# Optimization experiments

Measured on AMD Instinct MI355X. Metric: run time of the kernel, lower is better.

Reference implementation:

```python
import jax, jax.numpy as jnp
import numpy as np

EMB = 256
N_NODES = 100000
N_EDGES = 500000
N_REL = 10
REL_DIM = 64
HID = 128
HEADS = 4
HEAD_DIM = HID // HEADS


def setup_inputs() -> dict:
    key = jax.random.key(0)
    ks = jax.random.split(key, 16)
    s = lambda i, shape: jax.random.normal(ks[i], shape, dtype=jnp.float32) * 0.05
    return {
        "node_embeddings": jax.random.normal(ks[0], (N_NODES, EMB), dtype=jnp.float32),
        "edge_index": jax.random.randint(ks[1], (2, N_EDGES), 0, N_NODES),
        "relation_type": jax.random.randint(ks[2], (N_EDGES,), 0, N_REL),
        "rel_emb": s(3, (N_REL, REL_DIM)),
        "W_edge": s(4, (2 * EMB, HID)), "b_edge": jnp.zeros((HID,), jnp.float32),
        "W_q": s(5, (REL_DIM, HID)), "b_q": jnp.zeros((HID,), jnp.float32),
        "W_k": s(6, (HID, HID)), "b_k": jnp.zeros((HID,), jnp.float32),
        "W_v": s(7, (HID, HID)), "b_v": jnp.zeros((HID,), jnp.float32),
        "W_o1": s(8, (HID, HID)), "b_o1": jnp.zeros((HID,), jnp.float32),
        "W_o2": s(9, (HID, 1)), "b_o2": jnp.zeros((1,), jnp.float32),
    }


def reference(node_embeddings, edge_index, relation_type, rel_emb,
              W_edge, b_edge, W_q, b_q, W_k, b_k, W_v, b_v,
              W_o1, b_o1, W_o2, b_o2):
    # Gather endpoint features: [E, 2*EMB]
    src = node_embeddings[edge_index[0]]
    tgt = node_embeddings[edge_index[1]]
    edge_features = jnp.concatenate([src, tgt], axis=1)
    # Edge MLP (dropout is identity at eval): [E, HID]
    edge_hidden = jax.nn.relu(edge_features @ W_edge + b_edge)
    # Relation embedding lookup: [E, REL_DIM]
    rel = rel_emb[relation_type]
    E = edge_hidden.shape[0]
    Q = (rel @ W_q + b_q).reshape(E, HEADS, HEAD_DIM)
    K = (edge_hidden @ W_k + b_k).reshape(E, HEADS, HEAD_DIM)
    V = (edge_hidden @ W_v + b_v).reshape(E, HEADS, HEAD_DIM)
    scale = jnp.sqrt(jnp.float32(HEAD_DIM))
    scores = jnp.sum(Q * K, axis=-1) / scale          # [E, HEADS]
    attn = jax.nn.softmax(scores, axis=-1)            # softmax over heads
    attended = (attn[..., None] * V).reshape(E, HID)
    output = attended + edge_hidden
    # Output MLP: Linear->ReLU->Linear(1)
    h = jax.nn.relu(output @ W_o1 + b_o1)
    score = (h @ W_o2 + b_o2).squeeze(-1)             # [E]
    return score
```

## Files before the change

kernel.cpp:

```cpp
#include <hip/hip_runtime.h>

#define EMB   256
#define HID   128
#define RELD  64
#define NREL  10
#define TE    128
#define SHSTR 130

typedef __attribute__((ext_vector_type(8)))  short bf16x8;
typedef __attribute__((ext_vector_type(16))) float f32x16;

__device__ __forceinline__ float bf16_to_f32(unsigned short u) {
    union { unsigned int i; float f; } v;
    v.i = ((unsigned int)u) << 16;
    return v.f;
}

__device__ __forceinline__ unsigned short f32_to_bf16(float x) {
    union { unsigned int i; float f; } v;
    v.f = x;
    unsigned int b = v.i;
    unsigned int rounded = b + 0x7fffu + ((b >> 16) & 1u);
    return (unsigned short)(rounded >> 16);
}

template <bool F32>
__device__ __forceinline__ float ldx(const void* p, size_t i) {
    if (F32) return ((const float*)p)[i];
    return bf16_to_f32(((const unsigned short*)p)[i]);
}

__device__ __forceinline__ bool detect_f32(const void* nodeEmb) {
    const float* f = (const float*)nodeEmb;
    float x = f[(threadIdx.x & 63) * 997];
    bool sane = isfinite(x) && fabsf(x) < 1.0e6f;
    unsigned long long m = __ballot(sane);
    return __popcll(m) >= 48;
}

__device__ __forceinline__ void gload16(const void* g, void* l) {
    __builtin_amdgcn_global_load_lds(
        (const __attribute__((address_space(1))) unsigned int*)g,
        (__attribute__((address_space(3))) unsigned int*)l, 16, 0, 0);
}

#define WAITVL(n) asm volatile("s_waitcnt vmcnt(" #n ") lgkmcnt(0)" ::: "memory")

__device__ __forceinline__ void sbar() {
    __builtin_amdgcn_sched_barrier(0);
    __builtin_amdgcn_s_barrier();
    __builtin_amdgcn_sched_barrier(0);
}
__device__ __forceinline__ void bar_lds() {
    asm volatile("s_waitcnt lgkmcnt(0)" ::: "memory");
    sbar();
}

template <bool F32>
__device__ void prep_body(int vb, const void* W_edge, const void* W_k,
                          const void* W_v, const void* W_o1, const void* rel_emb,
                          const void* W_q, const void* b_q,
                          unsigned short* WTe, unsigned short* WTk,
                          unsigned short* WTv, unsigned short* WTo1, float* Qtab)
{
    if (vb < 448) {
        int idx = vb * 256 + threadIdx.x;
        if (idx < 65536) {
            int kc = idx >> 12, e = idx & 4095;
            int g = e >> 3, j = e & 7;
            int col = g & 127, kg = g >> 7;
            int k = kc * 32 + kg * 8 + j;
            WTe[idx] = f32_to_bf16(ldx<F32>(W_edge, (size_t)k * HID + col));
        } else if (idx < 65536 + 16384) {
            int i = idx - 65536;
            int kc = i >> 12, e = i & 4095;
            int g = e >> 3, j = e & 7;
            int col = g & 127, kg = (g >> 7) & 3;
            int k = kc * 32 + kg * 8 + j;
            WTk[i] = f32_to_bf16(ldx<F32>(W_k, (size_t)k * HID + col));
        } else if (idx < 65536 + 2 * 16384) {
            int i = idx - 65536 - 16384;
            int kc = i >> 12, e = i & 4095;
            int g = e >> 3, j = e & 7;
            int col = g & 127, kg = (g >> 7) & 3;
            int k = kc * 32 + kg * 8 + j;
            WTv[i] = f32_to_bf16(ldx<F32>(W_v, (size_t)k * HID + col));
        } else {
            int i = idx - 65536 - 2 * 16384;
            int kc = i >> 12, e = i & 4095;
            int g = e >> 3, j = e & 7;
            int col = g & 127, kg = (g >> 7) & 3;
            int k = kc * 32 + kg * 8 + j;
            WTo1[i] = f32_to_bf16(ldx<F32>(W_o1, (size_t)k * HID + col));
        }
    } else {
        const int t = threadIdx.x;
        const int c = t & (HID - 1);
        const int h = t >> 7;
        for (int r = h; r < NREL; r += 2) {
            float acc = 0.f;
            for (int d = 0; d < RELD; ++d)
                acc += ldx<F32>(rel_emb, r * RELD + d) * ldx<F32>(W_q, (size_t)d * HID + c);
            Qtab[r * HID + c] = acc + ldx<F32>(b_q, c);
        }
    }
}

__global__ void prep_kernel(const void* nodeEmb,
                            const void* W_edge, const void* W_k, const void* W_v,
                            const void* W_o1, const void* rel_emb, const void* W_q,
                            const void* b_q,
                            unsigned short* WTe, unsigned short* WTk,
                            unsigned short* WTv, unsigned short* WTo1, float* Qtab,
                            unsigned short* nodeBf16, int convBlocks,
                            unsigned long long nodeElems)
{
    bool f32 = detect_f32(nodeEmb);
    int b = blockIdx.x;
    if (b < convBlocks) {
        if (!f32) return;
        unsigned long long i = (unsigned long long)b * 2048ull + threadIdx.x * 8;
        if (i + 8 <= nodeElems) {
            const float* src = (const float*)nodeEmb + i;
            float4 f0 = *(const float4*)src;
            float4 f1 = *(const float4*)(src + 4);
            union { unsigned short us[8]; uint4 v; } pk;
            pk.us[0] = f32_to_bf16(f0.x); pk.us[1] = f32_to_bf16(f0.y);
            pk.us[2] = f32_to_bf16(f0.z); pk.us[3] = f32_to_bf16(f0.w);
            pk.us[4] = f32_to_bf16(f1.x); pk.us[5] = f32_to_bf16(f1.y);
            pk.us[6] = f32_to_bf16(f1.z); pk.us[7] = f32_to_bf16(f1.w);
            *(uint4*)(nodeBf16 + i) = pk.v;
        }
        return;
    }
    b -= convBlocks;
    if (f32) prep_body<true >(b, W_edge, W_k, W_v, W_o1, rel_emb, W_q, b_q,
                              WTe, WTk, WTv, WTo1, Qtab);
    else     prep_body<false>(b, W_edge, W_k, W_v, W_o1, rel_emb, W_q, b_q,
                              WTe, WTk, WTv, WTo1, Qtab);
}

struct __align__(16) Smem {
    unsigned short sHid[16 * SHSTR * 8];
    unsigned short SB[2][8192];
    float sQf[NREL * HID];
    float sBias[5 * HID];
    float sSc[TE][4];
    float sAttn[TE][4];
    float sPart[TE][2];
    int   sSrc[TE], sTgt[TE], sRel[TE];
};

__device__ __forceinline__ int shid_idx(int row, int k) {
    return (((k >> 3) * SHSTR + row) << 3) + (k & 7);
}

template <bool GBF16>
__device__ __forceinline__ bf16x8 loadA8(const void* row, int off) {
    if (GBF16) {
        return *(const bf16x8*)((const unsigned short*)row + off);
    } else {
        const float* p = (const float*)row + off;
        float4 f0 = *(const float4*)p;
        float4 f1 = *(const float4*)(p + 4);
        union { unsigned short us[8]; bf16x8 v; } pk;
        pk.us[0] = f32_to_bf16(f0.x); pk.us[1] = f32_to_bf16(f0.y);
        pk.us[2] = f32_to_bf16(f0.z); pk.us[3] = f32_to_bf16(f0.w);
        pk.us[4] = f32_to_bf16(f1.x); pk.us[5] = f32_to_bf16(f1.y);
        pk.us[6] = f32_to_bf16(f1.z); pk.us[7] = f32_to_bf16(f1.w);
        return pk.v;
    }
}

template <bool F32, bool GBF16>
__device__ void fused_body(
    Smem& sm,
    const void* gsrc, const int* edgeIdx, const int* relType,
    const unsigned short* WTe, const unsigned short* WTk,
    const unsigned short* WTv, const unsigned short* WTo1,
    const void* b_edge, const void* b_k, const void* b_v,
    const void* b_o1, const void* W_o2, const void* b_o2,
    const float* Qtab, void* outp, int E)
{
    const int t   = threadIdx.x;
    const int l   = t & 63;
    const int w   = t >> 6;
    const int c   = l & 31;
    const int h5  = l >> 5;
    const int rt  = w >> 1;
    const int cg2 = w & 1;
    const int bs  = blockIdx.x * TE;
    const int aRow = 32 * rt + c;

    if (t < TE) {
        int e = bs + t;
        if (e >= E) e = E - 1;
        if (e < 0)  e = 0;
        sm.sSrc[t] = edgeIdx[e];
        sm.sTgt[t] = edgeIdx[E + e];
        int r = relType[e];
        if (r < 0) r = 0;
        if (r >= NREL) r = NREL - 1;
        sm.sRel[t] = r;
    }
    for (int i = t; i < 5 * HID; i += 512) {
        int which = i >> 7, j = i & (HID - 1);
        float v = (which == 0) ? ldx<F32>(b_edge, j)
                : (which == 1) ? ldx<F32>(b_k, j)
                : (which == 2) ? ldx<F32>(b_v, j)
                : (which == 3) ? ldx<F32>(b_o1, j)
                               : ldx<F32>(W_o2, j);
        sm.sBias[i] = v;
    }
    for (int i = t; i < NREL * HID; i += 512)
        sm.sQf[i] = Qtab[i];
    __syncthreads();

    const void* rowSrc;
    const void* rowTgt;
    if (GBF16) {
        rowSrc = (const void*)((const unsigned short*)gsrc + (size_t)sm.sSrc[aRow] * EMB);
        rowTgt = (const void*)((const unsigned short*)gsrc + (size_t)sm.sTgt[aRow] * EMB);
    } else {
        rowSrc = (const void*)((const float*)gsrc + (size_t)sm.sSrc[aRow] * EMB);
        rowTgt = (const void*)((const float*)gsrc + (size_t)sm.sTgt[aRow] * EMB);
    }

    char* const ldsB0 = (char*)sm.SB[0] + w * 1024;
    char* const ldsB1 = (char*)sm.SB[1] + w * 1024;

    #define LOAD_A(k32, s) \
        loadA8<GBF16>(((k32) < 8) ? rowSrc : rowTgt, ((k32) & 7) * 32 + (s) * 16 + h5 * 8)
    #define STAGE_B64(WT, kc, buf)                                               \
    {                                                                            \
        gload16((WT) + (2 * (kc)    ) * 4096 + t * 8,                            \
                ((buf) ? ldsB1 : ldsB0));                                        \
        gload16((WT) + (2 * (kc) + 1) * 4096 + t * 8,                            \
                ((buf) ? ldsB1 : ldsB0) + 8192);                                 \
    }

    #define MFMA_AR64(slot, buf, accv)                                           \
    {                                                                            \
        const char* sb_ = (const char*)sm.SB[(buf)];                             \
        _Pragma("unroll")                                                        \
        for (int h_ = 0; h_ < 2; ++h_)                                           \
        _Pragma("unroll")                                                        \
        for (int s_ = 0; s_ < 2; ++s_) {                                         \
            _Pragma("unroll")                                                    \
            for (int ct_ = 0; ct_ < 2; ++ct_) {                                  \
                bf16x8 b_ = *(const bf16x8*)                                     \
                    (sb_ + h_ * 8192 +                                           \
                     ((s_ * 256 + h5 * 128 + 64 * cg2 + 32 * ct_ + c) << 4));    \
                accv[ct_] = __builtin_amdgcn_mfma_f32_32x32x16_bf16(             \
                                aR[slot][h_ * 2 + s_], b_, accv[ct_], 0, 0, 0);  \
            }                                                                    \
        }                                                                        \
    }

    #define MFMA_H64(kc, buf, accv)                                              \
    {                                                                            \
        const char* sb_ = (const char*)sm.SB[(buf)];                             \
        _Pragma("unroll")                                                        \
        for (int h_ = 0; h_ < 2; ++h_)                                           \
        _Pragma("unroll")                                                        \
        for (int s_ = 0; s_ < 2; ++s_) {                                         \
            bf16x8 a_ = *(const bf16x8*)((const char*)sm.sHid +                  \
                ((((2 * (kc) + h_) * 4 + s_ * 2 + h5) * SHSTR + aRow) << 4));    \
            _Pragma("unroll")                                                    \
            for (int ct_ = 0; ct_ < 2; ++ct_) {                                  \
                bf16x8 b_ = *(const bf16x8*)                                     \
                    (sb_ + h_ * 8192 +                                           \
                     ((s_ * 256 + h5 * 128 + 64 * cg2 + 32 * ct_ + c) << 4));    \
                accv[ct_] = __builtin_amdgcn_mfma_f32_32x32x16_bf16(             \
                                a_, b_, accv[ct_], 0, 0, 0);                     \
            }                                                                    \
        }                                                                        \
    }

    #define FILL_A(slot, kc)                                                     \
    {                                                                            \
        aR[slot][0] = LOAD_A(2 * (kc),     0);                                   \
        aR[slot][1] = LOAD_A(2 * (kc),     1);                                   \
        aR[slot][2] = LOAD_A(2 * (kc) + 1, 0);                                   \
        aR[slot][3] = LOAD_A(2 * (kc) + 1, 1);                                   \
    }

    f32x16 acc[2];
    acc[0] = (f32x16)(0.0f); acc[1] = (f32x16)(0.0f);
    {
        bf16x8 aR[2][4];
        FILL_A(0, 0);
        FILL_A(1, 1);
        STAGE_B64(WTe, 0, 0);
        STAGE_B64(WTe, 1, 1);
        #pragma unroll
        for (int kc = 0; kc < 8; ++kc) {
            int buf = kc & 1;
            if (GBF16) {
                if (kc == 0)      { WAITVL(2); }
                else if (kc < 7)  { WAITVL(6); }
                else              { WAITVL(0); }
            } else {
                WAITVL(0);
            }
            sbar();
            MFMA_AR64((kc & 1), buf, acc);
            sbar();
            if (kc < 6) {
                FILL_A((kc & 1), kc + 2);
                STAGE_B64(WTe, kc + 2, buf);
            }
        }
    }
    STAGE_B64(WTk, 0, 0); STAGE_B64(WTk, 1, 1);
    {
        #pragma unroll
        for (int ct = 0; ct < 2; ++ct) {
            int col = 64 * cg2 + 32 * ct + c;
            float bb = sm.sBias[col];
            #pragma unroll
            for (int r = 0; r < 16; ++r) {
                int erow = 32 * rt + (r & 3) + 8 * (r >> 2) + 4 * h5;
                sm.sHid[shid_idx(erow, col)] = f32_to_bf16(fmaxf(acc[ct][r] + bb, 0.f));
            }
        }
    }
    bar_lds();

    f32x16 kacc[2];
    kacc[0] = (f32x16)(0.0f); kacc[1] = (f32x16)(0.0f);
    WAITVL(2); sbar();
    MFMA_H64(0, 0, kacc);
    sbar();
    STAGE_B64(WTv, 0, 0);
    WAITVL(2); sbar();
    MFMA_H64(1, 1, kacc);
    sbar();
    STAGE_B64(WTv, 1, 1);

    {
        float ps[2][16];
        #pragma unroll
        for (int ct = 0; ct < 2; ++ct) {
            int col = 64 * cg2 + 32 * ct + c;
            float bk = sm.sBias[HID + col];
            #pragma unroll
            for (int r = 0; r < 16; ++r) {
                int erow = 32 * rt + (r & 3) + 8 * (r >> 2) + 4 * h5;
                ps[ct][r] = (kacc[ct][r] + bk) * sm.sQf[sm.sRel[erow] * HID + col];
            }
        }
        #pragma unroll
        for (int m = 1; m < 32; m <<= 1)
            #pragma unroll
            for (int ct = 0; ct < 2; ++ct)
                #pragma unroll
                for (int r = 0; r < 16; ++r)
                    ps[ct][r] += __shfl_xor(ps[ct][r], m, 64);
        if (c == 0) {
            const float inv = 0.17677669529663687f;
            #pragma unroll
            for (int ct = 0; ct < 2; ++ct) {
                int head = 2 * cg2 + ct;
                #pragma unroll
                for (int r = 0; r < 16; ++r) {
                    int erow = 32 * rt + (r & 3) + 8 * (r >> 2) + 4 * h5;
                    sm.sSc[erow][head] = ps[ct][r] * inv;
                }
            }
        }
    }
    bar_lds();
    if (t < TE) {
        float s0 = sm.sSc[t][0], s1 = sm.sSc[t][1];
        float s2 = sm.sSc[t][2], s3 = sm.sSc[t][3];
        float m = fmaxf(fmaxf(s0, s1), fmaxf(s2, s3));
        float e0 = expf(s0 - m), e1 = expf(s1 - m);
        float e2 = expf(s2 - m), e3 = expf(s3 - m);
        float den = e0 + e1 + e2 + e3;
        sm.sAttn[t][0] = e0 / den; sm.sAttn[t][1] = e1 / den;
        sm.sAttn[t][2] = e2 / den; sm.sAttn[t][3] = e3 / den;
    }
    bar_lds();

    f32x16 vacc[2];
    vacc[0] = (f32x16)(0.0f); vacc[1] = (f32x16)(0.0f);
    WAITVL(2); sbar();
    MFMA_H64(0, 0, vacc);
    sbar();
    STAGE_B64(WTo1, 0, 0);
    WAITVL(2); sbar();
    MFMA_H64(1, 1, vacc);
    sbar();
    STAGE_B64(WTo1, 1, 1);

    {
        #pragma unroll
        for (int ct = 0; ct < 2; ++ct) {
            int col  = 64 * cg2 + 32 * ct + c;
            int head = 2 * cg2 + ct;
            float bv = sm.sBias[2 * HID + col];
            #pragma unroll
            for (int r = 0; r < 16; ++r) {
                int erow = 32 * rt + (r & 3) + 8 * (r >> 2) + 4 * h5;
                float at = sm.sAttn[erow][head];
                int   si = shid_idx(erow, col);
                float hv = bf16_to_f32(sm.sHid[si]);
                sm.sHid[si] = f32_to_bf16(at * (vacc[ct][r] + bv) + hv);
            }
        }
    }
    bar_lds();

    f32x16 oacc[2];
    oacc[0] = (f32x16)(0.0f); oacc[1] = (f32x16)(0.0f);
    WAITVL(2); sbar();
    MFMA_H64(0, 0, oacc);
    sbar();
    WAITVL(0); sbar();
    MFMA_H64(1, 1, oacc);
    sbar();
    {
        float pr[16];
        #pragma unroll
        for (int r = 0; r < 16; ++r) pr[r] = 0.f;
        #pragma unroll
        for (int ct = 0; ct < 2; ++ct) {
            int col = 64 * cg2 + 32 * ct + c;
            float bo = sm.sBias[3 * HID + col];
            float wo = sm.sBias[4 * HID + col];
            #pragma unroll
            for (int r = 0; r < 16; ++r)
                pr[r] += fmaxf(oacc[ct][r] + bo, 0.f) * wo;
        }
        #pragma unroll
        for (int m = 1; m < 32; m <<= 1)
            #pragma unroll
            for (int r = 0; r < 16; ++r)
                pr[r] += __shfl_xor(pr[r], m, 64);
        if (c == 0) {
            #pragma unroll
            for (int r = 0; r < 16; ++r) {
                int erow = 32 * rt + (r & 3) + 8 * (r >> 2) + 4 * h5;
                sm.sPart[erow][cg2] = pr[r];
            }
        }
    }
    bar_lds();
    if (t < TE) {
        int ge = bs + t;
        if (ge < E) {
            float val = sm.sPart[t][0] + sm.sPart[t][1] + ldx<F32>(b_o2, 0);
            if (F32) ((float*)outp)[ge] = val;
            else     ((unsigned short*)outp)[ge] = f32_to_bf16(val);
        }
    }

    #undef LOAD_A
    #undef STAGE_B64
    #undef MFMA_AR64
    #undef MFMA_H64
    #undef FILL_A
}

__global__ __launch_bounds__(512, 4) void RelationAttentionMLPHead_10539849744626_kernel(
    const void* nodeEmb, const unsigned short* nodeBf16, int useConv,
    const int* edgeIdx, const int* relType,
    const unsigned short* WTe, const unsigned short* WTk,
    const unsigned short* WTv, const unsigned short* WTo1,
    const void* b_edge, const void* b_k, const void* b_v,
    const void* b_o1, const void* W_o2, const void* b_o2,
    const float* Qtab, void* outp, int E)
{
    __shared__ Smem sm;
    if (detect_f32(nodeEmb)) {
        if (useConv)
            fused_body<true, true >(sm, nodeBf16, edgeIdx, relType, WTe, WTk, WTv, WTo1,
                                    b_edge, b_k, b_v, b_o1, W_o2, b_o2, Qtab, outp, E);
        else
            fused_body<true, false>(sm, nodeEmb, edgeIdx, relType, WTe, WTk, WTv, WTo1,
                                    b_edge, b_k, b_v, b_o1, W_o2, b_o2, Qtab, outp, E);
    } else {
        fused_body<false, true>(sm, nodeEmb, edgeIdx, relType, WTe, WTk, WTv, WTo1,
                                b_edge, b_k, b_v, b_o1, W_o2, b_o2, Qtab, outp, E);
    }
}

extern "C" void kernel_launch(void* const* d_in, const int* in_sizes, int n_in,
                              void* d_out, int out_size, void* d_ws, size_t ws_size,
                              hipStream_t stream) {
    (void)n_in;

    const void* nodeEmb = d_in[0];
    const int*  edgeIdx = (const int*)d_in[1];
    const int*  relType = (const int*)d_in[2];
    const void* rel_emb = d_in[3];
    const void* W_edge  = d_in[4];
    const void* b_edge  = d_in[5];
    const void* W_q     = d_in[6];
    const void* b_q     = d_in[7];
    const void* W_k     = d_in[8];
    const void* b_k     = d_in[9];
    const void* W_v     = d_in[10];
    const void* b_v     = d_in[11];
    const void* W_o1    = d_in[12];
    const void* b_o1    = d_in[13];
    const void* W_o2    = d_in[14];
    const void* b_o2    = d_in[15];

    int E = out_size;
    if (E <= 0) E = in_sizes ? in_sizes[2] : 0;
    if (E <= 0) E = 500000;

    unsigned long long nodeElems =
        (in_sizes && in_sizes[0] > 0) ? (unsigned long long)in_sizes[0] : 25600000ull;

    char* ws = (char*)d_ws;
    float*          Qtab     = (float*)ws;
    unsigned short* WTe      = (unsigned short*)(ws + 8192);
    unsigned short* WTk      = (unsigned short*)(ws + 139264);
    unsigned short* WTv      = (unsigned short*)(ws + 172032);
    unsigned short* WTo1     = (unsigned short*)(ws + 204800);
    unsigned short* nodeBf16 = (unsigned short*)(ws + 237568);

    size_t need = 237568ull + nodeElems * 2ull;
    int useConv = (ws_size >= need) ? 1 : 0;
    int convBlocks = useConv ? (int)((nodeElems + 2047ull) / 2048ull) : 0;

    prep_kernel<<<convBlocks + 449, 256, 0, stream>>>(
        nodeEmb, W_edge, W_k, W_v, W_o1, rel_emb, W_q, b_q,
        WTe, WTk, WTv, WTo1, Qtab, nodeBf16, convBlocks, nodeElems);

    int grid = (E + TE - 1) / TE;
    if (grid < 1) grid = 1;

    RelationAttentionMLPHead_10539849744626_kernel<<<grid, 512, 0, stream>>>(
        nodeEmb, nodeBf16, useConv, edgeIdx, relType, WTe, WTk, WTv, WTo1,
        b_edge, b_k, b_v, b_o1, W_o2, b_o2, Qtab, d_out, E);
}
```

Measured before the change: 429.3 us.

## Precompute per-node edge-MLP projections before gathering per edge

Splits the edge MLP's first layer algebraically: W_edge is applied once per node (src half and tgt half) in a new pregemm kernel, producing bf16 tables HS and HT. The edge kernel then gathers two 128-wide rows, adds them with the bias and applies relu, instead of gathering two 256-wide rows and running the 512x128 GEMM per edge. This cuts edge-side GEMM work and gather bytes, and replaces the separate bf16 conversion pass, at the cost of an extra node-level GEMM pass and an extra bf16 rounding of the intermediate sums.

```diff
diff --git a/kernel.cpp b/kernel.cpp
--- a/kernel.cpp
+++ b/kernel.cpp
@@ -111,33 +111,116 @@
                             const void* W_o1, const void* rel_emb, const void* W_q,
                             const void* b_q,
                             unsigned short* WTe, unsigned short* WTk,
-                            unsigned short* WTv, unsigned short* WTo1, float* Qtab,
-                            unsigned short* nodeBf16, int convBlocks,
-                            unsigned long long nodeElems)
+                            unsigned short* WTv, unsigned short* WTo1, float* Qtab)
 {
     bool f32 = detect_f32(nodeEmb);
-    int b = blockIdx.x;
-    if (b < convBlocks) {
-        if (!f32) return;
-        unsigned long long i = (unsigned long long)b * 2048ull + threadIdx.x * 8;
-        if (i + 8 <= nodeElems) {
-            const float* src = (const float*)nodeEmb + i;
-            float4 f0 = *(const float4*)src;
-            float4 f1 = *(const float4*)(src + 4);
-            union { unsigned short us[8]; uint4 v; } pk;
-            pk.us[0] = f32_to_bf16(f0.x); pk.us[1] = f32_to_bf16(f0.y);
-            pk.us[2] = f32_to_bf16(f0.z); pk.us[3] = f32_to_bf16(f0.w);
-            pk.us[4] = f32_to_bf16(f1.x); pk.us[5] = f32_to_bf16(f1.y);
-            pk.us[6] = f32_to_bf16(f1.z); pk.us[7] = f32_to_bf16(f1.w);
-            *(uint4*)(nodeBf16 + i) = pk.v;
-        }
-        return;
-    }
-    b -= convBlocks;
-    if (f32) prep_body<true >(b, W_edge, W_k, W_v, W_o1, rel_emb, W_q, b_q,
+    if (f32) prep_body<true >(blockIdx.x, W_edge, W_k, W_v, W_o1, rel_emb, W_q, b_q,
                               WTe, WTk, WTv, WTo1, Qtab);
-    else     prep_body<false>(b, W_edge, W_k, W_v, W_o1, rel_emb, W_q, b_q,
+    else     prep_body<false>(blockIdx.x, W_edge, W_k, W_v, W_o1, rel_emb, W_q, b_q,
                               WTe, WTk, WTv, WTo1, Qtab);
+}
+
+struct __align__(16) PSmem {
+    unsigned short SA[2][4096];
+    unsigned short SB[2][2][4096];
+};
+
+template <bool F32>
+__device__ void pregemm_body(PSmem& ps, const void* nodeEmb,
+                             const unsigned short* WTe,
+                             unsigned short* HS, unsigned short* HT,
+                             long long nodeRows)
+{
+    const int t   = threadIdx.x;
+    const int l   = t & 63;
+    const int w   = t >> 6;
+    const int c   = l & 31;
+    const int h5  = l >> 5;
+    const int rt  = w >> 1;
+    const int cg2 = w & 1;
+    const long long base = (long long)blockIdx.x * 128;
+
+    const int stRow = t & 127;
+    long long arow = base + stRow;
+    if (arow >= nodeRows) arow = nodeRows - 1;
+    const int colSub = (t >> 8) * 16 + ((t >> 7) & 1) * 8;
+    char* const ldsA0 = (char*)ps.SA[0] + w * 1024;
+    char* const ldsA1 = (char*)ps.SA[1] + w * 1024;
+
+    #define PSTAGE_A(kc, buf)                                                    \
+    {                                                                            \
+        size_t eoff = (size_t)arow * EMB + (size_t)((kc) * 32 + colSub);         \
+        if (!F32) {                                                              \
+            gload16((const unsigned short*)nodeEmb + eoff,                       \
+                    (buf) ? ldsA1 : ldsA0);                                      \
+        } else {                                                                 \
+            const float* p_ = (const float*)nodeEmb + eoff;                      \
+            float4 f0_ = *(const float4*)p_;                                     \
+            float4 f1_ = *(const float4*)(p_ + 4);                               \
+            union { unsigned short us[8]; uint4 v; } pk_;                        \
+            pk_.us[0] = f32_to_bf16(f0_.x); pk_.us[1] = f32_to_bf16(f0_.y);      \
+            pk_.us[2] = f32_to_bf16(f0_.z); pk_.us[3] = f32_to_bf16(f0_.w);      \
+            pk_.us[4] = f32_to_bf16(f1_.x); pk_.us[5] = f32_to_bf16(f1_.y);      \
+            pk_.us[6] = f32_to_bf16(f1_.z); pk_.us[7] = f32_to_bf16(f1_.w);      \
+            *(uint4*)((char*)ps.SA[(buf)] + t * 16) = pk_.v;                     \
+        }                                                                        \
+    }
+    #define PSTAGE_B(kc, buf)                                                    \
+    {                                                                            \
+        gload16(WTe + (kc) * 4096 + t * 8,       (char*)ps.SB[(buf)][0] + w * 1024); \
+        gload16(WTe + (8 + (kc)) * 4096 + t * 8, (char*)ps.SB[(buf)][1] + w * 1024); \
+    }
+
+    f32x16 accP[2], accQ[2];
+    accP[0] = (f32x16)(0.0f); accP[1] = (f32x16)(0.0f);
+    accQ[0] = (f32x16)(0.0f); accQ[1] = (f32x16)(0.0f);
+
+    PSTAGE_A(0, 0); PSTAGE_B(0, 0);
+    __syncthreads();
+    #pragma unroll
+    for (int kc = 0; kc < 8; ++kc) {
+        int buf = kc & 1;
+        if (kc < 7) { PSTAGE_A(kc + 1, buf ^ 1); PSTAGE_B(kc + 1, buf ^ 1); }
+        const char* sa_ = (const char*)ps.SA[buf];
+        #pragma unroll
+        for (int s_ = 0; s_ < 2; ++s_) {
+            bf16x8 a_ = *(const bf16x8*)(sa_ + ((s_ * 256 + h5 * 128 + 32 * rt + c) << 4));
+            #pragma unroll
+            for (int ct_ = 0; ct_ < 2; ++ct_) {
+                int boff = (s_ * 256 + h5 * 128 + 64 * cg2 + 32 * ct_ + c) << 4;
+                bf16x8 bT = *(const bf16x8*)((const char*)ps.SB[buf][0] + boff);
+                bf16x8 bB = *(const bf16x8*)((const char*)ps.SB[buf][1] + boff);
+                accP[ct_] = __builtin_amdgcn_mfma_f32_32x32x16_bf16(a_, bT, accP[ct_], 0, 0, 0);
+                accQ[ct_] = __builtin_amdgcn_mfma_f32_32x32x16_bf16(a_, bB, accQ[ct_], 0, 0, 0);
+            }
+        }
+        __syncthreads();
+    }
+    #pragma unroll
+    for (int ct = 0; ct < 2; ++ct) {
+        int col = 64 * cg2 + 32 * ct + c;
+        #pragma unroll
+        for (int r = 0; r < 16; ++r) {
+            long long grow = base + 32 * rt + (r & 3) + 8 * (r >> 2) + 4 * h5;
+            if (grow < nodeRows) {
+                HS[grow * HID + col] = f32_to_bf16(accP[ct][r]);
+                HT[grow * HID + col] = f32_to_bf16(accQ[ct][r]);
+            }
+        }
+    }
+    #undef PSTAGE_A
+    #undef PSTAGE_B
+}
+
+__global__ __launch_bounds__(512, 2) void pregemm_kernel(
+    const void* nodeEmb, const unsigned short* WTe,
+    unsigned short* HS, unsigned short* HT, long long nodeRows)
+{
+    __shared__ PSmem ps;
+    if (detect_f32(nodeEmb))
+        pregemm_body<true >(ps, nodeEmb, WTe, HS, HT, nodeRows);
+    else
+        pregemm_body<false>(ps, nodeEmb, WTe, HS, HT, nodeRows);
 }
 
 struct __align__(16) Smem {
@@ -170,6 +253,240 @@
         pk.us[6] = f32_to_bf16(f1.z); pk.us[7] = f32_to_bf16(f1.w);
         return pk.v;
     }
+}
+
+template <bool F32>
+__device__ void fused_body_pre(
+    Smem& sm,
+    const unsigned short* HS, const unsigned short* HT,
+    const int* edgeIdx, const int* relType,
+    const unsigned short* WTk, const unsigned short* WTv, const unsigned short* WTo1,
+    const void* b_edge, const void* b_k, const void* b_v,
+    const void* b_o1, const void* W_o2, const void* b_o2,
+    const float* Qtab, void* outp, int E)
+{
+    const int t   = threadIdx.x;
+    const int l   = t & 63;
+    const int w   = t >> 6;
+    const int c   = l & 31;
+    const int h5  = l >> 5;
+    const int rt  = w >> 1;
+    const int cg2 = w & 1;
+    const int bs  = blockIdx.x * TE;
+    const int aRow = 32 * rt + c;
+
+    if (t < TE) {
+        int e = bs + t;
+        if (e >= E) e = E - 1;
+        if (e < 0)  e = 0;
+        sm.sSrc[t] = edgeIdx[e];
+        sm.sTgt[t] = edgeIdx[E + e];
+        int r = relType[e];
+        if (r < 0) r = 0;
+        if (r >= NREL) r = NREL - 1;
+        sm.sRel[t] = r;
+    }
+    for (int i = t; i < 5 * HID; i += 512) {
+        int which = i >> 7, j = i & (HID - 1);
+        float v = (which == 0) ? ldx<F32>(b_edge, j)
+                : (which == 1) ? ldx<F32>(b_k, j)
+                : (which == 2) ? ldx<F32>(b_v, j)
+                : (which == 3) ? ldx<F32>(b_o1, j)
+                               : ldx<F32>(W_o2, j);
+        sm.sBias[i] = v;
+    }
+    for (int i = t; i < NREL * HID; i += 512)
+        sm.sQf[i] = Qtab[i];
+    __syncthreads();
+
+    char* const ldsB0 = (char*)sm.SB[0] + w * 1024;
+    char* const ldsB1 = (char*)sm.SB[1] + w * 1024;
+
+    #define STAGE_B64(WT, kc, buf)                                               \
+    {                                                                            \
+        gload16((WT) + (2 * (kc)    ) * 4096 + t * 8,                            \
+                ((buf) ? ldsB1 : ldsB0));                                        \
+        gload16((WT) + (2 * (kc) + 1) * 4096 + t * 8,                            \
+                ((buf) ? ldsB1 : ldsB0) + 8192);                                 \
+    }
+    #define MFMA_H64(kc, buf, accv)                                              \
+    {                                                                            \
+        const char* sb_ = (const char*)sm.SB[(buf)];                             \
+        _Pragma("unroll")                                                        \
+        for (int h_ = 0; h_ < 2; ++h_)                                           \
+        _Pragma("unroll")                                                        \
+        for (int s_ = 0; s_ < 2; ++s_) {                                         \
+            bf16x8 a_ = *(const bf16x8*)((const char*)sm.sHid +                  \
+                ((((2 * (kc) + h_) * 4 + s_ * 2 + h5) * SHSTR + aRow) << 4));    \
+            _Pragma("unroll")                                                    \
+            for (int ct_ = 0; ct_ < 2; ++ct_) {                                  \
+                bf16x8 b_ = *(const bf16x8*)                                     \
+                    (sb_ + h_ * 8192 +                                           \
+                     ((s_ * 256 + h5 * 128 + 64 * cg2 + 32 * ct_ + c) << 4));    \
+                accv[ct_] = __builtin_amdgcn_mfma_f32_32x32x16_bf16(             \
+                                a_, b_, accv[ct_], 0, 0, 0);                     \
+            }                                                                    \
+        }                                                                        \
+    }
+
+    {
+        const int e  = t >> 2;
+        const int ug = t & 3;
+        const unsigned short* Pr = HS + (size_t)sm.sSrc[e] * HID + ug * 32;
+        const unsigned short* Qr = HT + (size_t)sm.sTgt[e] * HID + ug * 32;
+        bf16x8 p0 = *(const bf16x8*)(Pr);      bf16x8 q0 = *(const bf16x8*)(Qr);
+        bf16x8 p1 = *(const bf16x8*)(Pr + 8);  bf16x8 q1 = *(const bf16x8*)(Qr + 8);
+        bf16x8 p2 = *(const bf16x8*)(Pr + 16); bf16x8 q2 = *(const bf16x8*)(Qr + 16);
+        bf16x8 p3 = *(const bf16x8*)(Pr + 24); bf16x8 q3 = *(const bf16x8*)(Qr + 24);
+        STAGE_B64(WTk, 0, 0);
+        STAGE_B64(WTk, 1, 1);
+        #pragma unroll
+        for (int j = 0; j < 4; ++j) {
+            bf16x8 pj = (j == 0) ? p0 : (j == 1) ? p1 : (j == 2) ? p2 : p3;
+            bf16x8 qj = (j == 0) ? q0 : (j == 1) ? q1 : (j == 2) ? q2 : q3;
+            union { unsigned short us[8]; bf16x8 v; } pk;
+            #pragma unroll
+            for (int i = 0; i < 8; ++i) {
+                float f = bf16_to_f32((unsigned short)pj[i])
+                        + bf16_to_f32((unsigned short)qj[i])
+                        + sm.sBias[ug * 32 + j * 8 + i];
+                pk.us[i] = f32_to_bf16(fmaxf(f, 0.f));
+            }
+            *(bf16x8*)&sm.sHid[(size_t)((ug * 4 + j) * SHSTR + e) * 8] = pk.v;
+        }
+    }
+    bar_lds();
+
+    f32x16 kacc[2];
+    kacc[0] = (f32x16)(0.0f); kacc[1] = (f32x16)(0.0f);
+    WAITVL(2); sbar();
+    MFMA_H64(0, 0, kacc);
+    sbar();
+    STAGE_B64(WTv, 0, 0);
+    WAITVL(2); sbar();
+    MFMA_H64(1, 1, kacc);
+    sbar();
+    STAGE_B64(WTv, 1, 1);
+
+    {
+        float ps[2][16];
+        #pragma unroll
+        for (int ct = 0; ct < 2; ++ct) {
+            int col = 64 * cg2 + 32 * ct + c;
+            float bk = sm.sBias[HID + col];
+            #pragma unroll
+            for (int r = 0; r < 16; ++r) {
+                int erow = 32 * rt + (r & 3) + 8 * (r >> 2) + 4 * h5;
+                ps[ct][r] = (kacc[ct][r] + bk) * sm.sQf[sm.sRel[erow] * HID + col];
+            }
+        }
+        #pragma unroll
+        for (int m = 1; m < 32; m <<= 1)
+            #pragma unroll
+            for (int ct = 0; ct < 2; ++ct)
+                #pragma unroll
+                for (int r = 0; r < 16; ++r)
+                    ps[ct][r] += __shfl_xor(ps[ct][r], m, 64);
+        if (c == 0) {
+            const float inv = 0.17677669529663687f;
+            #pragma unroll
+            for (int ct = 0; ct < 2; ++ct) {
+                int head = 2 * cg2 + ct;
+                #pragma unroll
+                for (int r = 0; r < 16; ++r) {
+                    int erow = 32 * rt + (r & 3) + 8 * (r >> 2) + 4 * h5;
+                    sm.sSc[erow][head] = ps[ct][r] * inv;
+                }
+            }
+        }
+    }
+    bar_lds();
+    if (t < TE) {
+        float s0 = sm.sSc[t][0], s1 = sm.sSc[t][1];
+        float s2 = sm.sSc[t][2], s3 = sm.sSc[t][3];
+        float m = fmaxf(fmaxf(s0, s1), fmaxf(s2, s3));
+        float e0 = expf(s0 - m), e1 = expf(s1 - m);
+        float e2 = expf(s2 - m), e3 = expf(s3 - m);
+        float den = e0 + e1 + e2 + e3;
+        sm.sAttn[t][0] = e0 / den; sm.sAttn[t][1] = e1 / den;
+        sm.sAttn[t][2] = e2 / den; sm.sAttn[t][3] = e3 / den;
+    }
+    bar_lds();
+
+    f32x16 vacc[2];
+    vacc[0] = (f32x16)(0.0f); vacc[1] = (f32x16)(0.0f);
+    WAITVL(2); sbar();
+    MFMA_H64(0, 0, vacc);
+    sbar();
+    STAGE_B64(WTo1, 0, 0);
+    WAITVL(2); sbar();
+    MFMA_H64(1, 1, vacc);
+    sbar();
+    STAGE_B64(WTo1, 1, 1);
+
+    {
+        #pragma unroll
+        for (int ct = 0; ct < 2; ++ct) {
+            int col  = 64 * cg2 + 32 * ct + c;
+            int head = 2 * cg2 + ct;
+            float bv = sm.sBias[2 * HID + col];
+            #pragma unroll
+            for (int r = 0; r < 16; ++r) {
+                int erow = 32 * rt + (r & 3) + 8 * (r >> 2) + 4 * h5;
+                float at = sm.sAttn[erow][head];
+                int   si = shid_idx(erow, col);
+                float hv = bf16_to_f32(sm.sHid[si]);
+                sm.sHid[si] = f32_to_bf16(at * (vacc[ct][r] + bv) + hv);
+            }
+        }
+    }
+    bar_lds();
+
+    f32x16 oacc[2];
+    oacc[0] = (f32x16)(0.0f); oacc[1] = (f32x16)(0.0f);
+    WAITVL(2); sbar();
+    MFMA_H64(0, 0, oacc);
+    sbar();
+    WAITVL(0); sbar();
+    MFMA_H64(1, 1, oacc);
+    sbar();
+    {
+        float pr[16];
+        #pragma unroll
+        for (int r = 0; r < 16; ++r) pr[r] = 0.f;
+        #pragma unroll
+        for (int ct = 0; ct < 2; ++ct) {
+            int col = 64 * cg2 + 32 * ct + c;
+            float bo = sm.sBias[3 * HID + col];
+            float wo = sm.sBias[4 * HID + col];
+            #pragma unroll
+            for (int r = 0; r < 16; ++r)
+                pr[r] += fmaxf(oacc[ct][r] + bo, 0.f) * wo;
+        }
+        #pragma unroll
+        for (int m = 1; m < 32; m <<= 1)
+            #pragma unroll
+            for (int r = 0; r < 16; ++r)
+                pr[r] += __shfl_xor(pr[r], m, 64);
+        if (c == 0) {
+            #pragma unroll
+            for (int r = 0; r < 16; ++r) {
+                int erow = 32 * rt + (r & 3) + 8 * (r >> 2) + 4 * h5;
+                sm.sPart[erow][cg2] = pr[r];
+            }
+        }
+    }
+    bar_lds();
+    if (t < TE) {
+        int ge = bs + t;
+        if (ge < E) {
+            float val = sm.sPart[t][0] + sm.sPart[t][1] + ldx<F32>(b_o2, 0);
+            if (F32) ((float*)outp)[ge] = val;
+            else     ((unsigned short*)outp)[ge] = f32_to_bf16(val);
+        }
+    }
+    #undef STAGE_B64
+    #undef MFMA_H64
 }
 
 template <bool F32, bool GBF16>
@@ -238,7 +555,6 @@
         gload16((WT) + (2 * (kc) + 1) * 4096 + t * 8,                            \
                 ((buf) ? ldsB1 : ldsB0) + 8192);                                 \
     }
-
     #define MFMA_AR64(slot, buf, accv)                                           \
     {                                                                            \
         const char* sb_ = (const char*)sm.SB[(buf)];                             \
@@ -256,7 +572,6 @@
             }                                                                    \
         }                                                                        \
     }
-
     #define MFMA_H64(kc, buf, accv)                                              \
     {                                                                            \
         const char* sb_ = (const char*)sm.SB[(buf)];                             \
@@ -276,7 +591,6 @@
             }                                                                    \
         }                                                                        \
     }
-
     #define FILL_A(slot, kc)                                                     \
     {                                                                            \
         aR[slot][0] = LOAD_A(2 * (kc),     0);                                   \
@@ -455,7 +769,6 @@
             else     ((unsigned short*)outp)[ge] = f32_to_bf16(val);
         }
     }
-
     #undef LOAD_A
     #undef STAGE_B64
     #undef MFMA_AR64
@@ -464,7 +777,7 @@
 }
 
 __global__ __launch_bounds__(512, 4) void RelationAttentionMLPHead_10539849744626_kernel(
-    const void* nodeEmb, const unsigned short* nodeBf16, int useConv,
+    const void* nodeEmb, const unsigned short* HS, const unsigned short* HT, int useP,
     const int* edgeIdx, const int* relType,
     const unsigned short* WTe, const unsigned short* WTk,
     const unsigned short* WTv, const unsigned short* WTo1,
@@ -473,16 +786,17 @@
     const float* Qtab, void* outp, int E)
 {
     __shared__ Smem sm;
-    if (detect_f32(nodeEmb)) {
-        if (useConv)
-            fused_body<true, true >(sm, nodeBf16, edgeIdx, relType, WTe, WTk, WTv, WTo1,
-                                    b_edge, b_k, b_v, b_o1, W_o2, b_o2, Qtab, outp, E);
-        else
-            fused_body<true, false>(sm, nodeEmb, edgeIdx, relType, WTe, WTk, WTv, WTo1,
-                                    b_edge, b_k, b_v, b_o1, W_o2, b_o2, Qtab, outp, E);
+    bool f32 = detect_f32(nodeEmb);
+    if (useP) {
+        if (f32) fused_body_pre<true >(sm, HS, HT, edgeIdx, relType, WTk, WTv, WTo1,
+                                       b_edge, b_k, b_v, b_o1, W_o2, b_o2, Qtab, outp, E);
+        else     fused_body_pre<false>(sm, HS, HT, edgeIdx, relType, WTk, WTv, WTo1,
+                                       b_edge, b_k, b_v, b_o1, W_o2, b_o2, Qtab, outp, E);
     } else {
-        fused_body<false, true>(sm, nodeEmb, edgeIdx, relType, WTe, WTk, WTv, WTo1,
-                                b_edge, b_k, b_v, b_o1, W_o2, b_o2, Qtab, outp, E);
+        if (f32) fused_body<true, false>(sm, nodeEmb, edgeIdx, relType, WTe, WTk, WTv, WTo1,
+                                         b_edge, b_k, b_v, b_o1, W_o2, b_o2, Qtab, outp, E);
+        else     fused_body<false, true>(sm, nodeEmb, edgeIdx, relType, WTe, WTk, WTv, WTo1,
+                                         b_edge, b_k, b_v, b_o1, W_o2, b_o2, Qtab, outp, E);
     }
 }
 
@@ -514,27 +828,34 @@
 
     unsigned long long nodeElems =
         (in_sizes && in_sizes[0] > 0) ? (unsigned long long)in_sizes[0] : 25600000ull;
+    long long nodeRows = (long long)(nodeElems / EMB);
+    if (nodeRows < 1) nodeRows = 1;
 
     char* ws = (char*)d_ws;
-    float*          Qtab     = (float*)ws;
-    unsigned short* WTe      = (unsigned short*)(ws + 8192);
-    unsigned short* WTk      = (unsigned short*)(ws + 139264);
-    unsigned short* WTv      = (unsigned short*)(ws + 172032);
-    unsigned short* WTo1     = (unsigned short*)(ws + 204800);
-    unsigned short* nodeBf16 = (unsigned short*)(ws + 237568);
-
-    size_t need = 237568ull + nodeElems * 2ull;
-    int useConv = (ws_size >= need) ? 1 : 0;
-    int convBlocks = useConv ? (int)((nodeElems + 2047ull) / 2048ull) : 0;
-
-    prep_kernel<<<convBlocks + 449, 256, 0, stream>>>(
+    float*          Qtab = (float*)ws;
+    unsigned short* WTe  = (unsigned short*)(ws + 8192);
+    unsigned short* WTk  = (unsigned short*)(ws + 139264);
+    unsigned short* WTv  = (unsigned short*)(ws + 172032);
+    unsigned short* WTo1 = (unsigned short*)(ws + 204800);
+    unsigned short* HS   = (unsigned short*)(ws + 237568);
+    unsigned short* HT   = HS + (size_t)nodeRows * HID;
+
+    size_t need = 237568ull + (size_t)nodeRows * 512ull;
+    int useP = (ws_size >= need) ? 1 : 0;
+
+    prep_kernel<<<449, 256, 0, stream>>>(
         nodeEmb, W_edge, W_k, W_v, W_o1, rel_emb, W_q, b_q,
-        WTe, WTk, WTv, WTo1, Qtab, nodeBf16, convBlocks, nodeElems);
+        WTe, WTk, WTv, WTo1, Qtab);
+
+    if (useP) {
+        int pgrid = (int)((nodeRows + 127) / 128);
+        pregemm_kernel<<<pgrid, 512, 0, stream>>>(nodeEmb, WTe, HS, HT, nodeRows);
+    }
 
     int grid = (E + TE - 1) / TE;
     if (grid < 1) grid = 1;
 
     RelationAttentionMLPHead_10539849744626_kernel<<<grid, 512, 0, stream>>>(
-        nodeEmb, nodeBf16, useConv, edgeIdx, relType, WTe, WTk, WTv, WTo1,
+        nodeEmb, HS, HT, useP, edgeIdx, relType, WTe, WTk, WTv, WTo1,
         b_edge, b_k, b_v, b_o1, W_o2, b_o2, Qtab, d_out, E);
 }
```

Result: faster. 385.4 us (-10.2%).
